# Optimization experiments

Measured on AMD Instinct MI355X. Metric: run time of the kernel, lower is better.

## Reference

```python
import jax, jax.numpy as jnp
import numpy as np

NSEG = 64          # static number of segments (labels in [0, NSEG))
MARGIN = 0.25
W_PUSH = 1.0
W_PULL = 0.1


def setup_inputs() -> dict:
    key = jax.random.key(0)
    k1, k2 = jax.random.split(key)
    preds = jax.random.normal(k1, (4, 2, 16, 512, 512), dtype=jnp.float32)
    labels = jax.random.randint(k2, (4, 1, 512, 512), 0, NSEG, dtype=jnp.int32)
    return {"preds": preds, "labels": labels}


def reference(preds, labels):
    B, S, D, H, W = preds.shape
    P = H * W
    tags = preds.reshape(B, S, D, P)      # [B, n_stack, tag_dim, P]
    seg = labels.reshape(B, P)            # [B, P]
    iu, ju = jnp.triu_indices(NSEG, k=1)  # static upper-triangular pairs

    def per_item(t, s):
        # t: [S, D, P], s: [P]
        # --- scatter-mean: per-segment centroids ---
        tt = t.reshape(S * D, P).T                               # [P, S*D]
        sums = jax.ops.segment_sum(tt, s, num_segments=NSEG)     # [NSEG, S*D]
        counts = jax.ops.segment_sum(jnp.ones((P,), t.dtype), s, num_segments=NSEG)
        cent = (sums / jnp.maximum(counts, 1.0)[:, None]).reshape(NSEG, S, D)
        c = jnp.transpose(cent, (1, 2, 0))                       # [S, D, NSEG]
        # --- push: pairwise L1-mean centroid distance, upper triangle ---
        dist = jnp.abs(c[:, :, :, None] - c[:, :, None, :]).mean(axis=1)  # [S, NSEG, NSEG]
        cd = dist[:, iu, ju]                                     # [S, NSEG*(NSEG-1)/2]
        push = jnp.mean(jax.nn.relu(MARGIN - cd) ** 2)
        # --- pull: gather centroids back to pixels ---
        pc = c[:, :, s]                                          # [S, D, P]
        d = jnp.abs(t - pc).mean(axis=1)                         # [S, P]
        pull = jnp.mean(d ** 2)
        return push, pull

    pushes, pulls = jax.vmap(per_item)(tags, seg)                # [B], [B]
    return (W_PUSH * pushes + W_PULL * pulls).mean()
```

## Files before the change

### kernel.cpp

```cpp
#include <hip/hip_runtime.h>
#include <hip/hip_bf16.h>

#define BB 4
#define SS 2
#define DD 16
#define CH 32
#define PP (512*512)
#define NSEGC 64
#define MARGINF 0.25f

#define CHUNK 1024
#define NCHUNK (PP/CHUNK)
#define PXP 2048
#define NCHKP (PP/PXP)
#define CSTR 33

typedef __attribute__((ext_vector_type(4))) float  f32x4;
typedef __attribute__((ext_vector_type(8))) short  short8;

__device__ inline short f2bf(float x) {
    union { __hip_bfloat16 h; short s; } u;
    u.h = __float2bfloat16(x);
    return u.s;
}

__global__ __launch_bounds__(256) void k_sums(const float* __restrict__ preds,
                                              const int* __restrict__ labels,
                                              float* __restrict__ g_sums,
                                              float* __restrict__ g_counts,
                                              unsigned short* __restrict__ t_bf)
{
    __shared__ int   labs[CHUNK];
    __shared__ float buf[4][CH][68];
    __shared__ float cbuf[4][NSEGC];

    const int b    = blockIdx.x / NCHUNK;
    const int base = (blockIdx.x % NCHUNK) * CHUNK;
    const int tid  = threadIdx.x;
    const int w    = tid >> 6;
    const int l    = tid & 63;
    const int lm   = l & 15;
    const int lk   = l >> 4;

    ((int4*)labs)[tid] = ((const int4*)(labels + (size_t)b * PP + base))[tid];

    f32x4 acc[4][2];
    f32x4 accc[4];
#pragma unroll
    for (int mt = 0; mt < 4; ++mt) {
        accc[mt] = f32x4{0.f, 0.f, 0.f, 0.f};
#pragma unroll
        for (int nt = 0; nt < 2; ++nt) acc[mt][nt] = f32x4{0.f, 0.f, 0.f, 0.f};
    }
    short8 ones;
#pragma unroll
    for (int j = 0; j < 8; ++j) ones[j] = (short)0x3F80;

    __syncthreads();

    const float* pb = preds + (size_t)b * CH * PP + base;
    unsigned short* tbw = t_bf + ((size_t)b * CH + lm) * PP + base;

#pragma unroll 2
    for (int c = 0; c < 8; ++c) {
        const int kbase = (w * 8 + c) * 32 + lk * 8;
        const int4 L0 = *(const int4*)&labs[kbase];
        const int4 L1 = *(const int4*)&labs[kbase + 4];
        const int labv[8] = {L0.x, L0.y, L0.z, L0.w, L1.x, L1.y, L1.z, L1.w};

        short8 af[4];
#pragma unroll
        for (int mt = 0; mt < 4; ++mt) {
            const int target = mt * 16 + lm;
#pragma unroll
            for (int j = 0; j < 8; ++j)
                af[mt][j] = (labv[j] == target) ? (short)0x3F80 : (short)0;
        }

#pragma unroll
        for (int nt = 0; nt < 2; ++nt) {
            const float* src = pb + (size_t)(nt * 16 + lm) * PP + kbase;
            const float4 v0 = ((const float4*)src)[0];
            const float4 v1 = ((const float4*)src)[1];
            short8 bf;
            bf[0] = f2bf(v0.x); bf[1] = f2bf(v0.y); bf[2] = f2bf(v0.z); bf[3] = f2bf(v0.w);
            bf[4] = f2bf(v1.x); bf[5] = f2bf(v1.y); bf[6] = f2bf(v1.z); bf[7] = f2bf(v1.w);
            *(short8*)(tbw + (size_t)(nt * 16) * PP + kbase) = bf;
#pragma unroll
            for (int mt = 0; mt < 4; ++mt)
                acc[mt][nt] = __builtin_amdgcn_mfma_f32_16x16x32_bf16(af[mt], bf, acc[mt][nt], 0, 0, 0);
        }
#pragma unroll
        for (int mt = 0; mt < 4; ++mt)
            accc[mt] = __builtin_amdgcn_mfma_f32_16x16x32_bf16(af[mt], ones, accc[mt], 0, 0, 0);
    }

#pragma unroll
    for (int mt = 0; mt < 4; ++mt) {
#pragma unroll
        for (int nt = 0; nt < 2; ++nt)
            *(f32x4*)&buf[w][nt * 16 + lm][mt * 16 + lk * 4] = acc[mt][nt];
        if (lm == 0)
            *(f32x4*)&cbuf[w][mt * 16 + lk * 4] = accc[mt];
    }
    __syncthreads();

    for (int i = tid; i < CH * NSEGC; i += 256) {
        const int col = i >> 6, row = i & 63;
        const float s = buf[0][col][row] + buf[1][col][row] + buf[2][col][row] + buf[3][col][row];
        atomicAdd(&g_sums[(size_t)b * CH * NSEGC + i], s);
    }
    if (tid < NSEGC)
        atomicAdd(&g_counts[b * NSEGC + tid],
                  cbuf[0][tid] + cbuf[1][tid] + cbuf[2][tid] + cbuf[3][tid]);
}

__global__ __launch_bounds__(256) void k_push(const float* __restrict__ g_sums,
                                              const float* __restrict__ g_counts,
                                              float* __restrict__ g_cent,
                                              float* __restrict__ g_push)
{
    __shared__ float centB[CH * NSEGC];
    __shared__ float red[4];
    const int b = blockIdx.x;
    const int tid = threadIdx.x;

    for (int i = tid; i < CH * NSEGC; i += 256) {
        const int ch = i >> 6, seg = i & 63;
        const float cnt = fmaxf(g_counts[b * NSEGC + seg], 1.0f);
        const float c = g_sums[(size_t)b * CH * NSEGC + i] / cnt;
        centB[i] = c;
        g_cent[(size_t)b * NSEGC * CH + seg * CH + ch] = c;
    }
    __syncthreads();

    float acc = 0.f;
    for (int t = tid; t < SS * 2016; t += 256) {
        const int s = t / 2016;
        int rem = t % 2016;
        int i = 0;
        while (rem >= 63 - i) { rem -= 63 - i; ++i; }
        const int j = i + 1 + rem;
        float dsum = 0.f;
#pragma unroll
        for (int d = 0; d < DD; ++d) {
            const int ch = s * DD + d;
            dsum += fabsf(centB[ch * NSEGC + i] - centB[ch * NSEGC + j]);
        }
        const float cd = dsum * (1.f / DD);
        const float r = fmaxf(MARGINF - cd, 0.f);
        acc += r * r;
    }
    for (int o = 32; o > 0; o >>= 1) acc += __shfl_down(acc, o, 64);
    if ((tid & 63) == 0) red[tid >> 6] = acc;
    __syncthreads();
    if (tid == 0)
        g_push[b] = (red[0] + red[1] + red[2] + red[3]) * (1.0f / (SS * 2016));
}

__global__ __launch_bounds__(256) void k_pull(const unsigned short* __restrict__ t_bf,
                                              const int* __restrict__ labels,
                                              const float* __restrict__ g_cent,
                                              float* __restrict__ g_pull,
                                              const float* __restrict__ g_push,
                                              unsigned* __restrict__ g_done,
                                              float* __restrict__ out)
{
    __shared__ float centL[NSEGC * CSTR];
    __shared__ float red[4];
    const int b    = blockIdx.x / NCHKP;
    const int base = (blockIdx.x % NCHKP) * PXP;
    const int tid  = threadIdx.x;

    for (int i = tid; i < NSEGC * CH; i += 256) {
        const int seg = i >> 5, ch = i & 31;
        centL[seg * CSTR + ch] = g_cent[(size_t)b * NSEGC * CH + i];
    }
    const int* lp = labels + (size_t)b * PP + base + tid * 8;
    const int4 L0 = ((const int4*)lp)[0];
    const int4 L1 = ((const int4*)lp)[1];
    const int coff[8] = {L0.x * CSTR, L0.y * CSTR, L0.z * CSTR, L0.w * CSTR,
                         L1.x * CSTR, L1.y * CSTR, L1.z * CSTR, L1.w * CSTR};
    __syncthreads();

    float a0[8], a1[8];
#pragma unroll
    for (int j = 0; j < 8; ++j) { a0[j] = 0.f; a1[j] = 0.f; }

    const unsigned short* tb = t_bf + (size_t)b * CH * PP + base + tid * 8;
#pragma unroll
    for (int ch = 0; ch < CH; ++ch) {
        const short8 tv = *(const short8*)(tb + (size_t)ch * PP);
#pragma unroll
        for (int j = 0; j < 8; ++j) {
            const float f = __uint_as_float(((unsigned)(unsigned short)tv[j]) << 16);
            const float d = fabsf(f - centL[coff[j] + ch]);
            if (ch < 16) a0[j] += d; else a1[j] += d;
        }
    }

    float total = 0.f;
#pragma unroll
    for (int j = 0; j < 8; ++j) {
        float q;
        q = a0[j] * (1.f / DD); total += q * q;
        q = a1[j] * (1.f / DD); total += q * q;
    }
    for (int o = 32; o > 0; o >>= 1) total += __shfl_down(total, o, 64);
    if ((tid & 63) == 0) red[tid >> 6] = total;
    __syncthreads();

    if (tid == 0) {
        atomicAdd(&g_pull[b], red[0] + red[1] + red[2] + red[3]);
        __threadfence();
        const unsigned prev = atomicAdd(g_done, 1u);
        if (prev == gridDim.x - 1) {
            float accf = 0.f;
            for (int bb = 0; bb < BB; ++bb) {
                const float pu = atomicAdd(&g_pull[bb], 0.0f);
                const float ph = g_push[bb];
                accf += ph + 0.1f * (pu * (1.0f / (SS * PP)));
            }
            out[0] = accf * (1.0f / BB);
        }
    }
}

extern "C" void kernel_launch(void* const* d_in, const int* in_sizes, int n_in,
                              void* d_out, int out_size, void* d_ws, size_t ws_size,
                              hipStream_t stream) {
    const float* preds  = (const float*)d_in[0];
    const int*   labels = (const int*)d_in[1];

    float* ws       = (float*)d_ws;
    float* g_sums   = ws;
    float* g_counts = g_sums + BB * CH * NSEGC;
    float* g_pull   = g_counts + BB * NSEGC;
    float* g_push   = g_pull + BB;
    unsigned* g_done = (unsigned*)(g_push + BB);
    float* g_cent   = (float*)(g_done + 1);
    unsigned short* t_bf = (unsigned short*)(ws + 16896);

    hipMemsetAsync(d_ws, 0,
                   (size_t)(BB * CH * NSEGC + BB * NSEGC + BB + BB + 1) * sizeof(float),
                   stream);

    k_sums<<<BB * NCHUNK, 256, 0, stream>>>(preds, labels, g_sums, g_counts, t_bf);
    k_push<<<BB, 256, 0, stream>>>(g_sums, g_counts, g_cent, g_push);
    k_pull<<<BB * NCHKP, 256, 0, stream>>>(t_bf, labels, g_cent, g_pull, g_push,
                                           g_done, (float*)d_out);
}
```

Measured before the change: 100.2 us.

## Stage bf16-converted preds through swizzled LDS tile for coalesced global access

```diff
diff --git a/kernel.cpp b/kernel.cpp
--- a/kernel.cpp
+++ b/kernel.cpp
@@ -17,6 +17,7 @@
 
 typedef __attribute__((ext_vector_type(4))) float  f32x4;
 typedef __attribute__((ext_vector_type(8))) short  short8;
+typedef __attribute__((ext_vector_type(4))) short  short4_t;
 
 __device__ inline short f2bf(float x) {
     union { __hip_bfloat16 h; short s; } u;
@@ -24,15 +25,16 @@
     return u.s;
 }
 
-__global__ __launch_bounds__(256) void k_sums(const float* __restrict__ preds,
-                                              const int* __restrict__ labels,
-                                              float* __restrict__ g_sums,
-                                              float* __restrict__ g_counts,
-                                              unsigned short* __restrict__ t_bf)
+__global__ __launch_bounds__(256, 4) void k_sums(const float* __restrict__ preds,
+                                                 const int* __restrict__ labels,
+                                                 float* __restrict__ g_sums,
+                                                 float* __restrict__ g_counts,
+                                                 unsigned short* __restrict__ t_bf)
 {
+    __shared__ float buf[4][CH][68];
     __shared__ int   labs[CHUNK];
-    __shared__ float buf[4][CH][68];
     __shared__ float cbuf[4][NSEGC];
+    unsigned short* tile = (unsigned short*)&buf[0][0][0];
 
     const int b    = blockIdx.x / NCHUNK;
     const int base = (blockIdx.x % NCHUNK) * CHUNK;
@@ -56,43 +58,55 @@
 #pragma unroll
     for (int j = 0; j < 8; ++j) ones[j] = (short)0x3F80;
 
-    __syncthreads();
-
-    const float* pb = preds + (size_t)b * CH * PP + base;
-    unsigned short* tbw = t_bf + ((size_t)b * CH + lm) * PP + base;
-
-#pragma unroll 2
-    for (int c = 0; c < 8; ++c) {
-        const int kbase = (w * 8 + c) * 32 + lk * 8;
-        const int4 L0 = *(const int4*)&labs[kbase];
-        const int4 L1 = *(const int4*)&labs[kbase + 4];
-        const int labv[8] = {L0.x, L0.y, L0.z, L0.w, L1.x, L1.y, L1.z, L1.w};
-
-        short8 af[4];
-#pragma unroll
-        for (int mt = 0; mt < 4; ++mt) {
-            const int target = mt * 16 + lm;
-#pragma unroll
-            for (int j = 0; j < 8; ++j)
-                af[mt][j] = (labv[j] == target) ? (short)0x3F80 : (short)0;
-        }
-
-#pragma unroll
-        for (int nt = 0; nt < 2; ++nt) {
-            const float* src = pb + (size_t)(nt * 16 + lm) * PP + kbase;
-            const float4 v0 = ((const float4*)src)[0];
-            const float4 v1 = ((const float4*)src)[1];
-            short8 bf;
-            bf[0] = f2bf(v0.x); bf[1] = f2bf(v0.y); bf[2] = f2bf(v0.z); bf[3] = f2bf(v0.w);
-            bf[4] = f2bf(v1.x); bf[5] = f2bf(v1.y); bf[6] = f2bf(v1.z); bf[7] = f2bf(v1.w);
-            *(short8*)(tbw + (size_t)(nt * 16) * PP + kbase) = bf;
+    const float*    pb  = preds + (size_t)b * CH * PP + base;
+    unsigned short* tbb = t_bf  + (size_t)b * CH * PP + base;
+
+#pragma unroll 1
+    for (int sc = 0; sc < 4; ++sc) {
+        const int px0 = sc * 256;
+#pragma unroll
+        for (int i = 0; i < 8; ++i) {
+            const int ch = w * 8 + i;
+            const float4 v = ((const float4*)(pb + (size_t)ch * PP + px0))[l];
+            short4_t s4;
+            s4[0] = f2bf(v.x); s4[1] = f2bf(v.y); s4[2] = f2bf(v.z); s4[3] = f2bf(v.w);
+            *(short4_t*)(tbb + (size_t)ch * PP + px0 + 4 * l) = s4;
+            const int g = (l >> 1) ^ (ch & 7);
+            *(short4_t*)&tile[ch * 256 + g * 8 + (l & 1) * 4] = s4;
+        }
+        __syncthreads();
+
+#pragma unroll
+        for (int cc = 0; cc < 2; ++cc) {
+            const int c  = 2 * w + cc;
+            const int kb = px0 + c * 32 + lk * 8;
+            const int4 L0 = *(const int4*)&labs[kb];
+            const int4 L1 = *(const int4*)&labs[kb + 4];
+            const int labv[8] = {L0.x, L0.y, L0.z, L0.w, L1.x, L1.y, L1.z, L1.w};
+
+            short8 af[4];
+#pragma unroll
+            for (int mt = 0; mt < 4; ++mt) {
+                const int target = mt * 16 + lm;
+#pragma unroll
+                for (int j = 0; j < 8; ++j)
+                    af[mt][j] = (labv[j] == target) ? (short)0x3F80 : (short)0;
+            }
+
+#pragma unroll
+            for (int nt = 0; nt < 2; ++nt) {
+                const int ch = nt * 16 + lm;
+                const int g  = (c * 4 + lk) ^ (ch & 7);
+                const short8 bf = *(const short8*)&tile[ch * 256 + g * 8];
+#pragma unroll
+                for (int mt = 0; mt < 4; ++mt)
+                    acc[mt][nt] = __builtin_amdgcn_mfma_f32_16x16x32_bf16(af[mt], bf, acc[mt][nt], 0, 0, 0);
+            }
 #pragma unroll
             for (int mt = 0; mt < 4; ++mt)
-                acc[mt][nt] = __builtin_amdgcn_mfma_f32_16x16x32_bf16(af[mt], bf, acc[mt][nt], 0, 0, 0);
-        }
-#pragma unroll
-        for (int mt = 0; mt < 4; ++mt)
-            accc[mt] = __builtin_amdgcn_mfma_f32_16x16x32_bf16(af[mt], ones, accc[mt], 0, 0, 0);
+                accc[mt] = __builtin_amdgcn_mfma_f32_16x16x32_bf16(af[mt], ones, accc[mt], 0, 0, 0);
+        }
+        __syncthreads();
     }
 
 #pragma unroll
```

After: 97.44 us. 1.03x faster.

## Fuse sum, push and pull into one cooperative kernel with grid sync

Applied to the files above, without the earlier changes.

```diff
diff --git a/kernel.cpp b/kernel.cpp
--- a/kernel.cpp
+++ b/kernel.cpp
@@ -1,5 +1,8 @@
 #include <hip/hip_runtime.h>
 #include <hip/hip_bf16.h>
+#include <hip/hip_cooperative_groups.h>
+
+namespace cg = cooperative_groups;
 
 #define BB 4
 #define SS 2
@@ -8,12 +11,12 @@
 #define PP (512*512)
 #define NSEGC 64
 #define MARGINF 0.25f
-
+#define CSTR 33
+
+#define PXF 2048
+#define NBF (PP/PXF)
 #define CHUNK 1024
 #define NCHUNK (PP/CHUNK)
-#define PXP 2048
-#define NCHKP (PP/PXP)
-#define CSTR 33
 
 typedef __attribute__((ext_vector_type(4))) float  f32x4;
 typedef __attribute__((ext_vector_type(8))) short  short8;
@@ -24,11 +27,195 @@
     return u.s;
 }
 
+__global__ __launch_bounds__(256, 2) void k_fused(const float* __restrict__ preds,
+                                                  const int* __restrict__ labels,
+                                                  float* __restrict__ g_sums,
+                                                  float* __restrict__ g_counts,
+                                                  float* __restrict__ g_pull,
+                                                  float* __restrict__ g_push,
+                                                  unsigned* __restrict__ g_done,
+                                                  float* __restrict__ out)
+{
+    __shared__ int   labs[PXF];
+    __shared__ float buf[4][CH][68];
+    __shared__ float cbuf[4][NSEGC];
+    __shared__ float centL[NSEGC * CSTR];
+    __shared__ float redP[4];
+    __shared__ float red[4];
+
+    const int b    = blockIdx.x >> 7;
+    const int base = (blockIdx.x & (NBF - 1)) * PXF;
+    const int tid  = threadIdx.x;
+    const int w    = tid >> 6;
+    const int l    = tid & 63;
+    const int lm   = l & 15;
+    const int lk   = l >> 4;
+
+    ((int4*)labs)[tid]       = ((const int4*)(labels + (size_t)b * PP + base))[tid];
+    ((int4*)labs)[256 + tid] = ((const int4*)(labels + (size_t)b * PP + base))[256 + tid];
+
+    f32x4 acc[4][2];
+    f32x4 accc[4];
+#pragma unroll
+    for (int mt = 0; mt < 4; ++mt) {
+        accc[mt] = f32x4{0.f, 0.f, 0.f, 0.f};
+#pragma unroll
+        for (int nt = 0; nt < 2; ++nt) acc[mt][nt] = f32x4{0.f, 0.f, 0.f, 0.f};
+    }
+    short8 ones;
+#pragma unroll
+    for (int j = 0; j < 8; ++j) ones[j] = (short)0x3F80;
+
+    __syncthreads();
+
+    const float* pb = preds + (size_t)b * CH * PP + base;
+
+#pragma unroll 2
+    for (int c = 0; c < 16; ++c) {
+        const int kbase = w * 512 + c * 32 + lk * 8;
+        const int4 L0 = *(const int4*)&labs[kbase];
+        const int4 L1 = *(const int4*)&labs[kbase + 4];
+        const int labv[8] = {L0.x, L0.y, L0.z, L0.w, L1.x, L1.y, L1.z, L1.w};
+
+        short8 af[4];
+#pragma unroll
+        for (int mt = 0; mt < 4; ++mt) {
+            const int target = mt * 16 + lm;
+#pragma unroll
+            for (int j = 0; j < 8; ++j)
+                af[mt][j] = (labv[j] == target) ? (short)0x3F80 : (short)0;
+        }
+
+#pragma unroll
+        for (int nt = 0; nt < 2; ++nt) {
+            const float* src = pb + (size_t)(nt * 16 + lm) * PP + kbase;
+            const float4 v0 = ((const float4*)src)[0];
+            const float4 v1 = ((const float4*)src)[1];
+            short8 bf;
+            bf[0] = f2bf(v0.x); bf[1] = f2bf(v0.y); bf[2] = f2bf(v0.z); bf[3] = f2bf(v0.w);
+            bf[4] = f2bf(v1.x); bf[5] = f2bf(v1.y); bf[6] = f2bf(v1.z); bf[7] = f2bf(v1.w);
+#pragma unroll
+            for (int mt = 0; mt < 4; ++mt)
+                acc[mt][nt] = __builtin_amdgcn_mfma_f32_16x16x32_bf16(af[mt], bf, acc[mt][nt], 0, 0, 0);
+        }
+#pragma unroll
+        for (int mt = 0; mt < 4; ++mt)
+            accc[mt] = __builtin_amdgcn_mfma_f32_16x16x32_bf16(af[mt], ones, accc[mt], 0, 0, 0);
+    }
+
+#pragma unroll
+    for (int mt = 0; mt < 4; ++mt) {
+#pragma unroll
+        for (int nt = 0; nt < 2; ++nt)
+            *(f32x4*)&buf[w][nt * 16 + lm][mt * 16 + lk * 4] = acc[mt][nt];
+        if (lm == 0)
+            *(f32x4*)&cbuf[w][mt * 16 + lk * 4] = accc[mt];
+    }
+    __syncthreads();
+
+    for (int i = tid; i < CH * NSEGC; i += 256) {
+        const int col = i >> 6, row = i & 63;
+        const float s = buf[0][col][row] + buf[1][col][row] + buf[2][col][row] + buf[3][col][row];
+        atomicAdd(&g_sums[(size_t)b * CH * NSEGC + i], s);
+    }
+    if (tid < NSEGC)
+        atomicAdd(&g_counts[b * NSEGC + tid],
+                  cbuf[0][tid] + cbuf[1][tid] + cbuf[2][tid] + cbuf[3][tid]);
+
+    __threadfence();
+    cg::this_grid().sync();
+
+    if (tid < NSEGC) cbuf[0][tid] = fmaxf(g_counts[b * NSEGC + tid], 1.0f);
+    __syncthreads();
+#pragma unroll
+    for (int k = 0; k < 8; ++k) {
+        const int idx = tid * 8 + k;
+        const int ch = idx >> 6, seg = idx & 63;
+        centL[seg * CSTR + ch] = g_sums[(size_t)b * CH * NSEGC + idx] / cbuf[0][seg];
+    }
+    __syncthreads();
+
+    if ((blockIdx.x & (NBF - 1)) == 0) {
+        float acc_p = 0.f;
+        for (int t = tid; t < SS * 2016; t += 256) {
+            const int s = t / 2016;
+            int rem = t % 2016;
+            int i = 0;
+            while (rem >= 63 - i) { rem -= 63 - i; ++i; }
+            const int j = i + 1 + rem;
+            float dsum = 0.f;
+#pragma unroll
+            for (int d = 0; d < DD; ++d) {
+                const int ch = s * DD + d;
+                dsum += fabsf(centL[i * CSTR + ch] - centL[j * CSTR + ch]);
+            }
+            const float cd = dsum * (1.f / DD);
+            const float r = fmaxf(MARGINF - cd, 0.f);
+            acc_p += r * r;
+        }
+        for (int o = 32; o > 0; o >>= 1) acc_p += __shfl_down(acc_p, o, 64);
+        if ((tid & 63) == 0) redP[tid >> 6] = acc_p;
+        __syncthreads();
+        if (tid == 0)
+            atomicAdd(&g_push[b], (redP[0] + redP[1] + redP[2] + redP[3]) * (1.0f / (SS * 2016)));
+    }
+
+    const int* lp = labels + (size_t)b * PP + base + tid * 8;
+    const int4 L0 = ((const int4*)lp)[0];
+    const int4 L1 = ((const int4*)lp)[1];
+    const int coff[8] = {L0.x * CSTR, L0.y * CSTR, L0.z * CSTR, L0.w * CSTR,
+                         L1.x * CSTR, L1.y * CSTR, L1.z * CSTR, L1.w * CSTR};
+
+    float a0[8], a1[8];
+#pragma unroll
+    for (int j = 0; j < 8; ++j) { a0[j] = 0.f; a1[j] = 0.f; }
+
+    const float* pbase = preds + (size_t)b * CH * PP + base + tid * 8;
+#pragma unroll
+    for (int ch = 0; ch < CH; ++ch) {
+        const float4 v0 = ((const float4*)(pbase + (size_t)ch * PP))[0];
+        const float4 v1 = ((const float4*)(pbase + (size_t)ch * PP))[1];
+        float* aa = (ch < 16) ? a0 : a1;
+        aa[0] += fabsf(v0.x - centL[coff[0] + ch]);
+        aa[1] += fabsf(v0.y - centL[coff[1] + ch]);
+        aa[2] += fabsf(v0.z - centL[coff[2] + ch]);
+        aa[3] += fabsf(v0.w - centL[coff[3] + ch]);
+        aa[4] += fabsf(v1.x - centL[coff[4] + ch]);
+        aa[5] += fabsf(v1.y - centL[coff[5] + ch]);
+        aa[6] += fabsf(v1.z - centL[coff[6] + ch]);
+        aa[7] += fabsf(v1.w - centL[coff[7] + ch]);
+    }
+    float total = 0.f;
+#pragma unroll
+    for (int j = 0; j < 8; ++j) {
+        float q;
+        q = a0[j] * (1.f / DD); total += q * q;
+        q = a1[j] * (1.f / DD); total += q * q;
+    }
+    for (int o = 32; o > 0; o >>= 1) total += __shfl_down(total, o, 64);
+    if ((tid & 63) == 0) red[tid >> 6] = total;
+    __syncthreads();
+
+    if (tid == 0) {
+        atomicAdd(&g_pull[b], red[0] + red[1] + red[2] + red[3]);
+        __threadfence();
+        const unsigned prev = atomicAdd(g_done, 1u);
+        if (prev == gridDim.x - 1) {
+            float accf = 0.f;
+            for (int bb = 0; bb < BB; ++bb) {
+                const float pu = atomicAdd(&g_pull[bb], 0.0f);
+                const float ph = atomicAdd(&g_push[bb], 0.0f);
+                accf += ph + 0.1f * (pu * (1.0f / (SS * PP)));
+            }
+            out[0] = accf * (1.0f / BB);
+        }
+    }
+}
+
 __global__ __launch_bounds__(256) void k_sums(const float* __restrict__ preds,
                                               const int* __restrict__ labels,
                                               float* __restrict__ g_sums,
-                                              float* __restrict__ g_counts,
-                                              unsigned short* __restrict__ t_bf)
+                                              float* __restrict__ g_counts)
 {
     __shared__ int   labs[CHUNK];
     __shared__ float buf[4][CH][68];
@@ -59,7 +246,6 @@
     __syncthreads();
 
     const float* pb = preds + (size_t)b * CH * PP + base;
-    unsigned short* tbw = t_bf + ((size_t)b * CH + lm) * PP + base;
 
 #pragma unroll 2
     for (int c = 0; c < 8; ++c) {
@@ -76,7 +262,6 @@
             for (int j = 0; j < 8; ++j)
                 af[mt][j] = (labv[j] == target) ? (short)0x3F80 : (short)0;
         }
-
 #pragma unroll
         for (int nt = 0; nt < 2; ++nt) {
             const float* src = pb + (size_t)(nt * 16 + lm) * PP + kbase;
@@ -85,7 +270,6 @@
             short8 bf;
             bf[0] = f2bf(v0.x); bf[1] = f2bf(v0.y); bf[2] = f2bf(v0.z); bf[3] = f2bf(v0.w);
             bf[4] = f2bf(v1.x); bf[5] = f2bf(v1.y); bf[6] = f2bf(v1.z); bf[7] = f2bf(v1.w);
-            *(short8*)(tbw + (size_t)(nt * 16) * PP + kbase) = bf;
 #pragma unroll
             for (int mt = 0; mt < 4; ++mt)
                 acc[mt][nt] = __builtin_amdgcn_mfma_f32_16x16x32_bf16(af[mt], bf, acc[mt][nt], 0, 0, 0);
@@ -158,18 +342,18 @@
         g_push[b] = (red[0] + red[1] + red[2] + red[3]) * (1.0f / (SS * 2016));
 }
 
-__global__ __launch_bounds__(256) void k_pull(const unsigned short* __restrict__ t_bf,
-                                              const int* __restrict__ labels,
-                                              const float* __restrict__ g_cent,
-                                              float* __restrict__ g_pull,
-                                              const float* __restrict__ g_push,
-                                              unsigned* __restrict__ g_done,
-                                              float* __restrict__ out)
+__global__ __launch_bounds__(256) void k_pull_fb(const float* __restrict__ preds,
+                                                 const int* __restrict__ labels,
+                                                 const float* __restrict__ g_cent,
+                                                 float* __restrict__ g_pull,
+                                                 const float* __restrict__ g_push,
+                                                 unsigned* __restrict__ g_done,
+                                                 float* __restrict__ out)
 {
     __shared__ float centL[NSEGC * CSTR];
     __shared__ float red[4];
-    const int b    = blockIdx.x / NCHKP;
-    const int base = (blockIdx.x % NCHKP) * PXP;
+    const int b    = blockIdx.x >> 7;
+    const int base = (blockIdx.x & (NBF - 1)) * PXF;
     const int tid  = threadIdx.x;
 
     for (int i = tid; i < NSEGC * CH; i += 256) {
@@ -187,18 +371,21 @@
 #pragma unroll
     for (int j = 0; j < 8; ++j) { a0[j] = 0.f; a1[j] = 0.f; }
 
-    const unsigned short* tb = t_bf + (size_t)b * CH * PP + base + tid * 8;
+    const float* pbase = preds + (size_t)b * CH * PP + base + tid * 8;
 #pragma unroll
     for (int ch = 0; ch < CH; ++ch) {
-        const short8 tv = *(const short8*)(tb + (size_t)ch * PP);
-#pragma unroll
-        for (int j = 0; j < 8; ++j) {
-            const float f = __uint_as_float(((unsigned)(unsigned short)tv[j]) << 16);
-            const float d = fabsf(f - centL[coff[j] + ch]);
-            if (ch < 16) a0[j] += d; else a1[j] += d;
-        }
-    }
-
+        const float4 v0 = ((const float4*)(pbase + (size_t)ch * PP))[0];
+        const float4 v1 = ((const float4*)(pbase + (size_t)ch * PP))[1];
+        float* aa = (ch < 16) ? a0 : a1;
+        aa[0] += fabsf(v0.x - centL[coff[0] + ch]);
+        aa[1] += fabsf(v0.y - centL[coff[1] + ch]);
+        aa[2] += fabsf(v0.z - centL[coff[2] + ch]);
+        aa[3] += fabsf(v0.w - centL[coff[3] + ch]);
+        aa[4] += fabsf(v1.x - centL[coff[4] + ch]);
+        aa[5] += fabsf(v1.y - centL[coff[5] + ch]);
+        aa[6] += fabsf(v1.z - centL[coff[6] + ch]);
+        aa[7] += fabsf(v1.w - centL[coff[7] + ch]);
+    }
     float total = 0.f;
 #pragma unroll
     for (int j = 0; j < 8; ++j) {
@@ -239,14 +426,20 @@
     float* g_push   = g_pull + BB;
     unsigned* g_done = (unsigned*)(g_push + BB);
     float* g_cent   = (float*)(g_done + 1);
-    unsigned short* t_bf = (unsigned short*)(ws + 16896);
+    float* outp     = (float*)d_out;
 
     hipMemsetAsync(d_ws, 0,
                    (size_t)(BB * CH * NSEGC + BB * NSEGC + BB + BB + 1) * sizeof(float),
                    stream);
 
-    k_sums<<<BB * NCHUNK, 256, 0, stream>>>(preds, labels, g_sums, g_counts, t_bf);
-    k_push<<<BB, 256, 0, stream>>>(g_sums, g_counts, g_cent, g_push);
-    k_pull<<<BB * NCHKP, 256, 0, stream>>>(t_bf, labels, g_cent, g_pull, g_push,
-                                           g_done, (float*)d_out);
-}
+    void* kargs[] = {(void*)&preds, (void*)&labels, (void*)&g_sums, (void*)&g_counts,
+                     (void*)&g_pull, (void*)&g_push, (void*)&g_done, (void*)&outp};
+    hipError_t e = hipLaunchCooperativeKernel((const void*)k_fused, dim3(BB * NBF), dim3(256),
+                                              kargs, 0, stream);
+    if (e != hipSuccess) {
+        k_sums   <<<BB * NCHUNK, 256, 0, stream>>>(preds, labels, g_sums, g_counts);
+        k_push   <<<BB, 256, 0, stream>>>(g_sums, g_counts, g_cent, g_push);
+        k_pull_fb<<<BB * NBF, 256, 0, stream>>>(preds, labels, g_cent, g_pull, g_push,
+                                                g_done, outp);
+    }
+}
```

Measured after the change: 149.2 us. +49.0%, slower.
